# Optimization experiments

Hardware: AMD Instinct MI355X
Metric: run time of the kernel (lower is better)

The kernel has to match this reference:

```python
import jax, jax.numpy as jnp
import numpy as np

N = 50000      # num nodes
HID = 64       # hidden_dim
N2V = 64       # node2vec dim
E = 800000     # num edges
EP = 100000    # prediction edges
L = 2          # num_layers
EPS = 1e-5     # BatchNorm eps


def setup_inputs() -> dict:
    key = jax.random.key(0)
    ks = jax.random.split(key, 8)
    edge_index = jax.random.randint(ks[0], (2, E), 0, N)
    pred_edge = jax.random.randint(ks[1], (EP, 2), 0, N)
    id_emb = jax.random.normal(ks[2], (N, HID), jnp.float32) * 0.1      # learnable ID embedding
    n2v_emb = jax.random.normal(ks[3], (N, N2V), jnp.float32) * 0.1     # frozen node2vec embedding
    proj_w = jax.random.normal(ks[4], (HID + N2V, HID), jnp.float32) / np.sqrt(HID + N2V)
    proj_b = jnp.zeros((HID,), jnp.float32)
    conv_w = jax.random.normal(ks[5], (L, HID, HID), jnp.float32) / np.sqrt(HID)
    conv_b = jnp.zeros((L, HID), jnp.float32)
    bn_gamma = jnp.ones((L, HID), jnp.float32)
    bn_beta = jnp.zeros((L, HID), jnp.float32)
    return {"edge_index": edge_index, "pred_edge": pred_edge, "id_emb": id_emb,
            "n2v_emb": n2v_emb, "proj_w": proj_w, "proj_b": proj_b,
            "conv_w": conv_w, "conv_b": conv_b, "bn_gamma": bn_gamma, "bn_beta": bn_beta}


def reference(edge_index, pred_edge, id_emb, n2v_emb, proj_w, proj_b, conv_w, conv_b, bn_gamma, bn_beta):
    # input projection of concatenated embeddings: [N, HID+N2V] @ [HID+N2V, HID]
    x = jnp.concatenate([id_emb, n2v_emb], axis=1) @ proj_w + proj_b

    # GCN normalization with self-loops: norm_e = d^-1/2[src] * d^-1/2[dst]
    loops = jnp.arange(N, dtype=edge_index.dtype)
    row = jnp.concatenate([edge_index[0], loops])   # source nodes
    col = jnp.concatenate([edge_index[1], loops])   # destination nodes
    deg = jax.ops.segment_sum(jnp.ones(row.shape, x.dtype), col, num_segments=N)
    dis = jnp.where(deg > 0, jax.lax.rsqrt(deg), 0.0)
    norm = dis[row] * dis[col]                      # [E+N]

    for l in range(L):
        h = x @ conv_w[l]                                                    # [N, HID]
        agg = jax.ops.segment_sum(norm[:, None] * h[row], col, num_segments=N) + conv_b[l]
        # BatchNorm1d (training-mode batch stats over nodes)
        mu = agg.mean(axis=0)
        var = agg.var(axis=0)
        xn = (agg - mu) * jax.lax.rsqrt(var + EPS) * bn_gamma[l] + bn_beta[l]
        x = x + jax.nn.relu(xn)                                              # residual (shapes match)

    # dot-product link decoder
    z = x
    return (z[pred_edge[:, 0]] * z[pred_edge[:, 1]]).sum(axis=1)
```

## Files before the change

### kernel.cpp

```cpp
#include <hip/hip_runtime.h>

#define NN 50000
#define HID 64
#define NE 800000
#define NP 100000
#define BN_EPS 1e-5f
#define NB1 196

static inline size_t alignup(size_t x) { return (x + 255) & ~(size_t)255; }

__device__ __forceinline__ void f4fma(float a, const float4& w, float4& c) {
    c.x += a * w.x; c.y += a * w.y; c.z += a * w.z; c.w += a * w.w;
}
__device__ __forceinline__ void f4add(const float4& a, float4& c) {
    c.x += a.x; c.y += a.y; c.z += a.z; c.w += a.w;
}
__device__ __forceinline__ unsigned bfpack(float a, float b) {
    unsigned ua = __float_as_uint(a), ub = __float_as_uint(b);
    ua = (ua + 0x7fffu + ((ua >> 16) & 1u)) >> 16;
    ub = (ub + 0x7fffu + ((ub >> 16) & 1u)) >> 16;
    return ua | (ub << 16);
}
__device__ __forceinline__ float4 bf2f4(uint2 u) {
    float4 r;
    r.x = __uint_as_float(u.x << 16);
    r.y = __uint_as_float(u.x & 0xffff0000u);
    r.z = __uint_as_float(u.y << 16);
    r.w = __uint_as_float(u.y & 0xffff0000u);
    return r;
}


__global__ __launch_bounds__(256) void k_zero(int* __restrict__ cnt, float* __restrict__ sums,
                                              int* __restrict__ cursor) {
    int i = blockIdx.x * blockDim.x + threadIdx.x;
    if (i < NN) cnt[i] = 0;
    if (i < 256) sums[i] = 0.f;
    if (i == 0) *cursor = 0;
}


__global__ __launch_bounds__(256) void k_count(const int* __restrict__ col,
                                               int* __restrict__ cnt, int* __restrict__ rank) {
    int e = blockIdx.x * blockDim.x + threadIdx.x;
    if (e < NE) rank[e] = atomicAdd(&cnt[col[e]], 1);
}


__global__ __launch_bounds__(256) void k_alloc(const int* __restrict__ cnt,
                                               int* __restrict__ offs,
                                               float* __restrict__ dis,
                                               int* __restrict__ cursor) {
    __shared__ int s[256];
    __shared__ int base;
    int t = threadIdx.x;
    int i = blockIdx.x * 256 + t;
    int v = (i < NN) ? cnt[i] : 0;
    if (i < NN) dis[i] = rsqrtf((float)(v + 1));
    s[t] = v;
    __syncthreads();
    for (int off = 1; off < 256; off <<= 1) {
        int add = (t >= off) ? s[t - off] : 0;
        __syncthreads();
        s[t] += add;
        __syncthreads();
    }
    if (t == 255) base = atomicAdd(cursor, s[255]);
    __syncthreads();
    if (i < NN) offs[i] = base + s[t] - v;
}


__global__ __launch_bounds__(256) void k_fill(const int* __restrict__ row, const int* __restrict__ col,
                                              const int* __restrict__ rank, const int* __restrict__ offs,
                                              int* __restrict__ csr_src) {
    int e = blockIdx.x * blockDim.x + threadIdx.x;
    if (e >= NE) return;
    csr_src[offs[col[e]] + rank[e]] = row[e];
}


__global__ __launch_bounds__(256) void k_proj(const float* __restrict__ id_emb,
                                              const float* __restrict__ n2v,
                                              const float* __restrict__ W,
                                              const float* __restrict__ b,
                                              const float* __restrict__ dis,
                                              float* __restrict__ x,
                                              unsigned short* __restrict__ xh) {
    __shared__ float Wl[128 * 64];
    int tid = threadIdx.x;
    for (int i = tid; i < 128 * 64; i += 256) Wl[i] = W[i];
    __syncthreads();
    int sub = tid >> 4, q = tid & 15;
    const float4* W4 = (const float4*)Wl;
    const float4* id4 = (const float4*)id_emb;
    const float4* nv4 = (const float4*)n2v;
    float4* x4 = (float4*)x;
    uint2* xh2 = (uint2*)xh;
    float4 bb = ((const float4*)b)[q];
    const int ngroups = (NN + 63) / 64;
    for (int g = blockIdx.x; g < ngroups; g += gridDim.x) {
        int n0 = g * 64 + sub * 4;
        int r0 = min(n0 + 0, NN - 1), r1 = min(n0 + 1, NN - 1);
        int r2 = min(n0 + 2, NN - 1), r3 = min(n0 + 3, NN - 1);
        float4 c0 = bb, c1 = bb, c2 = bb, c3 = bb;
#pragma unroll 4
        for (int k4 = 0; k4 < 16; ++k4) {
            float4 a0 = id4[r0 * 16 + k4];
            float4 a1 = id4[r1 * 16 + k4];
            float4 a2 = id4[r2 * 16 + k4];
            float4 a3 = id4[r3 * 16 + k4];
            float4 w0 = W4[(k4 * 4 + 0) * 16 + q];
            float4 w1 = W4[(k4 * 4 + 1) * 16 + q];
            float4 w2 = W4[(k4 * 4 + 2) * 16 + q];
            float4 w3 = W4[(k4 * 4 + 3) * 16 + q];
            f4fma(a0.x, w0, c0); f4fma(a0.y, w1, c0); f4fma(a0.z, w2, c0); f4fma(a0.w, w3, c0);
            f4fma(a1.x, w0, c1); f4fma(a1.y, w1, c1); f4fma(a1.z, w2, c1); f4fma(a1.w, w3, c1);
            f4fma(a2.x, w0, c2); f4fma(a2.y, w1, c2); f4fma(a2.z, w2, c2); f4fma(a2.w, w3, c2);
            f4fma(a3.x, w0, c3); f4fma(a3.y, w1, c3); f4fma(a3.z, w2, c3); f4fma(a3.w, w3, c3);
        }
#pragma unroll 4
        for (int k4 = 0; k4 < 16; ++k4) {
            float4 a0 = nv4[r0 * 16 + k4];
            float4 a1 = nv4[r1 * 16 + k4];
            float4 a2 = nv4[r2 * 16 + k4];
            float4 a3 = nv4[r3 * 16 + k4];
            float4 w0 = W4[(k4 * 4 + 64) * 16 + q];
            float4 w1 = W4[(k4 * 4 + 65) * 16 + q];
            float4 w2 = W4[(k4 * 4 + 66) * 16 + q];
            float4 w3 = W4[(k4 * 4 + 67) * 16 + q];
            f4fma(a0.x, w0, c0); f4fma(a0.y, w1, c0); f4fma(a0.z, w2, c0); f4fma(a0.w, w3, c0);
            f4fma(a1.x, w0, c1); f4fma(a1.y, w1, c1); f4fma(a1.z, w2, c1); f4fma(a1.w, w3, c1);
            f4fma(a2.x, w0, c2); f4fma(a2.y, w1, c2); f4fma(a2.z, w2, c2); f4fma(a2.w, w3, c2);
            f4fma(a3.x, w0, c3); f4fma(a3.y, w1, c3); f4fma(a3.z, w2, c3); f4fma(a3.w, w3, c3);
        }
        if (n0 + 0 < NN) { float d = dis[n0+0]; x4[(n0+0)*16+q] = c0;
            xh2[(n0+0)*16+q] = make_uint2(bfpack(c0.x*d,c0.y*d), bfpack(c0.z*d,c0.w*d)); }
        if (n0 + 1 < NN) { float d = dis[n0+1]; x4[(n0+1)*16+q] = c1;
            xh2[(n0+1)*16+q] = make_uint2(bfpack(c1.x*d,c1.y*d), bfpack(c1.z*d,c1.w*d)); }
        if (n0 + 2 < NN) { float d = dis[n0+2]; x4[(n0+2)*16+q] = c2;
            xh2[(n0+2)*16+q] = make_uint2(bfpack(c2.x*d,c2.y*d), bfpack(c2.z*d,c2.w*d)); }
        if (n0 + 3 < NN) { float d = dis[n0+3]; x4[(n0+3)*16+q] = c3;
            xh2[(n0+3)*16+q] = make_uint2(bfpack(c3.x*d,c3.y*d), bfpack(c3.z*d,c3.w*d)); }
    }
}


__global__ __launch_bounds__(256) void k_gg(const int* __restrict__ offs,
                                            const int* __restrict__ cnt,
                                            const int* __restrict__ csr_src,
                                            const float* __restrict__ dis,
                                            const unsigned short* __restrict__ xh,
                                            unsigned short* __restrict__ th,
                                            const float* __restrict__ W,
                                            float* __restrict__ agg,
                                            float* __restrict__ sums) {
    __shared__ float Wl[64 * 64];
    __shared__ float ls0[16][64];
    __shared__ float ls1[16][64];
    int tid = threadIdx.x;
    for (int i = tid; i < 64 * 64; i += 256) Wl[i] = W[i];
    int node0 = blockIdx.x * 64;
    const uint2* xh2 = (const uint2*)xh;
    uint2* th2 = (uint2*)th;
    {
        int wave = tid >> 6, lane = tid & 63;
        int gsub = lane >> 4, q = lane & 15;
        for (int r = 0; r < 4; ++r) {
            int node = node0 + wave * 16 + r * 4 + gsub;
            if (node < NN) {
                float4 acc = make_float4(0.f, 0.f, 0.f, 0.f);
                int j = offs[node], j1 = j + cnt[node];
                for (; j + 7 < j1; j += 8) {
                    int s0 = csr_src[j],     s1 = csr_src[j + 1], s2 = csr_src[j + 2], s3 = csr_src[j + 3];
                    int s4 = csr_src[j + 4], s5 = csr_src[j + 5], s6 = csr_src[j + 6], s7 = csr_src[j + 7];
                    uint2 u0 = xh2[s0 * 16 + q];
                    uint2 u1 = xh2[s1 * 16 + q];
                    uint2 u2 = xh2[s2 * 16 + q];
                    uint2 u3 = xh2[s3 * 16 + q];
                    uint2 u4 = xh2[s4 * 16 + q];
                    uint2 u5 = xh2[s5 * 16 + q];
                    uint2 u6 = xh2[s6 * 16 + q];
                    uint2 u7 = xh2[s7 * 16 + q];
                    f4add(bf2f4(u0), acc); f4add(bf2f4(u1), acc);
                    f4add(bf2f4(u2), acc); f4add(bf2f4(u3), acc);
                    f4add(bf2f4(u4), acc); f4add(bf2f4(u5), acc);
                    f4add(bf2f4(u6), acc); f4add(bf2f4(u7), acc);
                }
                for (; j < j1; ++j) {
                    uint2 u0 = xh2[csr_src[j] * 16 + q];
                    f4add(bf2f4(u0), acc);
                }
                f4add(bf2f4(xh2[node * 16 + q]), acc);
                float di = dis[node];
                acc.x *= di; acc.y *= di; acc.z *= di; acc.w *= di;
                th2[node * 16 + q] = make_uint2(bfpack(acc.x, acc.y), bfpack(acc.z, acc.w));
            }
        }
    }
    __syncthreads();
    int sub = tid >> 4, q = tid & 15;
    const uint2* t2 = (const uint2*)th;
    const float4* W4 = (const float4*)Wl;
    float4* agg4 = (float4*)agg;
    int n0 = node0 + sub * 4;
    int r0 = min(n0 + 0, NN - 1), r1 = min(n0 + 1, NN - 1);
    int r2 = min(n0 + 2, NN - 1), r3 = min(n0 + 3, NN - 1);
    float4 c0 = make_float4(0.f,0.f,0.f,0.f), c1 = c0, c2 = c0, c3 = c0;
#pragma unroll 4
    for (int k4 = 0; k4 < 16; ++k4) {
        float4 a0 = bf2f4(t2[r0 * 16 + k4]);
        float4 a1 = bf2f4(t2[r1 * 16 + k4]);
        float4 a2 = bf2f4(t2[r2 * 16 + k4]);
        float4 a3 = bf2f4(t2[r3 * 16 + k4]);
        float4 w0 = W4[(k4 * 4 + 0) * 16 + q];
        float4 w1 = W4[(k4 * 4 + 1) * 16 + q];
        float4 w2 = W4[(k4 * 4 + 2) * 16 + q];
        float4 w3 = W4[(k4 * 4 + 3) * 16 + q];
        f4fma(a0.x, w0, c0); f4fma(a0.y, w1, c0); f4fma(a0.z, w2, c0); f4fma(a0.w, w3, c0);
        f4fma(a1.x, w0, c1); f4fma(a1.y, w1, c1); f4fma(a1.z, w2, c1); f4fma(a1.w, w3, c1);
        f4fma(a2.x, w0, c2); f4fma(a2.y, w1, c2); f4fma(a2.z, w2, c2); f4fma(a2.w, w3, c2);
        f4fma(a3.x, w0, c3); f4fma(a3.y, w1, c3); f4fma(a3.z, w2, c3); f4fma(a3.w, w3, c3);
    }
    float4 s1 = make_float4(0.f,0.f,0.f,0.f), s2 = s1;
    if (n0 + 0 < NN) { agg4[(n0 + 0) * 16 + q] = c0;
        s1.x += c0.x; s1.y += c0.y; s1.z += c0.z; s1.w += c0.w;
        s2.x += c0.x*c0.x; s2.y += c0.y*c0.y; s2.z += c0.z*c0.z; s2.w += c0.w*c0.w; }
    if (n0 + 1 < NN) { agg4[(n0 + 1) * 16 + q] = c1;
        s1.x += c1.x; s1.y += c1.y; s1.z += c1.z; s1.w += c1.w;
        s2.x += c1.x*c1.x; s2.y += c1.y*c1.y; s2.z += c1.z*c1.z; s2.w += c1.w*c1.w; }
    if (n0 + 2 < NN) { agg4[(n0 + 2) * 16 + q] = c2;
        s1.x += c2.x; s1.y += c2.y; s1.z += c2.z; s1.w += c2.w;
        s2.x += c2.x*c2.x; s2.y += c2.y*c2.y; s2.z += c2.z*c2.z; s2.w += c2.w*c2.w; }
    if (n0 + 3 < NN) { agg4[(n0 + 3) * 16 + q] = c3;
        s1.x += c3.x; s1.y += c3.y; s1.z += c3.z; s1.w += c3.w;
        s2.x += c3.x*c3.x; s2.y += c3.y*c3.y; s2.z += c3.z*c3.z; s2.w += c3.w*c3.w; }
    ls0[sub][q * 4 + 0] = s1.x; ls0[sub][q * 4 + 1] = s1.y;
    ls0[sub][q * 4 + 2] = s1.z; ls0[sub][q * 4 + 3] = s1.w;
    ls1[sub][q * 4 + 0] = s2.x; ls1[sub][q * 4 + 1] = s2.y;
    ls1[sub][q * 4 + 2] = s2.z; ls1[sub][q * 4 + 3] = s2.w;
    __syncthreads();
    if (tid < 64) {
        float a = 0.f;
#pragma unroll
        for (int r = 0; r < 16; ++r) a += ls0[r][tid];
        atomicAdd(&sums[tid], a);
    } else if (tid < 128) {
        int c = tid - 64;
        float a = 0.f;
#pragma unroll
        for (int r = 0; r < 16; ++r) a += ls1[r][c];
        atomicAdd(&sums[64 + c], a);
    }
}


__global__ __launch_bounds__(256) void k_bnupdate(const float* __restrict__ agg,
                                                  const float* __restrict__ sums,
                                                  const float* __restrict__ gamma,
                                                  const float* __restrict__ beta,
                                                  const float* __restrict__ dis,
                                                  int prescale,
                                                  float* __restrict__ x,
                                                  unsigned short* __restrict__ xh) {
    int i = blockIdx.x * blockDim.x + threadIdx.x;
    if (i >= NN * 16) return;
    int f4 = i & 15;
    const float invn = 1.0f / (float)NN;
    float4 sm = ((const float4*)sums)[f4];
    float4 sq = ((const float4*)(sums + 64))[f4];
    float4 g = ((const float4*)gamma)[f4];
    float4 be = ((const float4*)beta)[f4];
    float4 a = ((const float4*)agg)[i];
    float4 xv = ((const float4*)x)[i];
    float mu, var, rstd, xn;
    mu = sm.x * invn; var = sq.x * invn - mu * mu; rstd = rsqrtf(var + BN_EPS);
    xn = (a.x - mu) * rstd * g.x + be.x; xv.x += fmaxf(xn, 0.f);
    mu = sm.y * invn; var = sq.y * invn - mu * mu; rstd = rsqrtf(var + BN_EPS);
    xn = (a.y - mu) * rstd * g.y + be.y; xv.y += fmaxf(xn, 0.f);
    mu = sm.z * invn; var = sq.z * invn - mu * mu; rstd = rsqrtf(var + BN_EPS);
    xn = (a.z - mu) * rstd * g.z + be.z; xv.z += fmaxf(xn, 0.f);
    mu = sm.w * invn; var = sq.w * invn - mu * mu; rstd = rsqrtf(var + BN_EPS);
    xn = (a.w - mu) * rstd * g.w + be.w; xv.w += fmaxf(xn, 0.f);
    ((float4*)x)[i] = xv;
    float d = prescale ? dis[i >> 4] : 1.0f;
    ((uint2*)xh)[i] = make_uint2(bfpack(xv.x * d, xv.y * d), bfpack(xv.z * d, xv.w * d));
}


__global__ __launch_bounds__(256) void k_decode(const int* __restrict__ pred,
                                                const unsigned short* __restrict__ zh,
                                                float* __restrict__ out) {
    int gw = (blockIdx.x * blockDim.x + threadIdx.x) >> 6;
    int lane = threadIdx.x & 63;
    int sub = lane >> 4, q = lane & 15;
    int p = gw * 4 + sub;
    if (p >= NP) return;
    const uint2* z2 = (const uint2*)zh;
    int a = pred[2 * p], b = pred[2 * p + 1];
    float4 va = bf2f4(z2[a * 16 + q]);
    float4 vb = bf2f4(z2[b * 16 + q]);
    float v = va.x * vb.x + va.y * vb.y + va.z * vb.z + va.w * vb.w;
    v += __shfl_xor(v, 1);
    v += __shfl_xor(v, 2);
    v += __shfl_xor(v, 4);
    v += __shfl_xor(v, 8);
    if (q == 0) out[p] = v;
}

extern "C" void kernel_launch(void* const* d_in, const int* in_sizes, int n_in,
                              void* d_out, int out_size, void* d_ws, size_t ws_size,
                              hipStream_t stream) {
    const int* edge_index = (const int*)d_in[0];
    const int* pred       = (const int*)d_in[1];
    const float* id_emb   = (const float*)d_in[2];
    const float* n2v      = (const float*)d_in[3];
    const float* proj_w   = (const float*)d_in[4];
    const float* proj_b   = (const float*)d_in[5];
    const float* conv_w   = (const float*)d_in[6];
    const float* gamma    = (const float*)d_in[8];
    const float* beta     = (const float*)d_in[9];
    float* out = (float*)d_out;

    char* ws = (char*)d_ws;
    size_t off = 0;
    float* dis   = (float*)(ws + off); off += alignup(NN * 4);
    int* cnt     = (int*)(ws + off);   off += alignup(NN * 4);
    int* offs    = (int*)(ws + off);   off += alignup(NN * 4);
    int* rank    = (int*)(ws + off);   off += alignup((size_t)NE * 4);
    int* cursor  = (int*)(ws + off);   off += alignup(4);
    int* csr_src = (int*)(ws + off);   off += alignup((size_t)NE * 4);
    float* x     = (float*)(ws + off); off += alignup((size_t)NN * 64 * 4);
    float* agg   = (float*)(ws + off); off += alignup((size_t)NN * 64 * 4);
    unsigned short* xh = (unsigned short*)(ws + off); off += alignup((size_t)NN * 64 * 2);
    unsigned short* th = (unsigned short*)(ws + off); off += alignup((size_t)NN * 64 * 2);
    float* sums  = (float*)(ws + off);

    const int* row = edge_index;
    const int* col = edge_index + NE;

    k_zero<<<NB1, 256, 0, stream>>>(cnt, sums, cursor);
    k_count<<<(NE + 255) / 256, 256, 0, stream>>>(col, cnt, rank);
    k_alloc<<<NB1, 256, 0, stream>>>(cnt, offs, dis, cursor);
    k_fill<<<(NE + 255) / 256, 256, 0, stream>>>(row, col, rank, offs, csr_src);

    k_proj<<<512, 256, 0, stream>>>(id_emb, n2v, proj_w, proj_b, dis, x, xh);

    for (int l = 0; l < 2; ++l) {
        k_gg<<<(NN + 63) / 64, 256, 0, stream>>>(offs, cnt, csr_src, dis, xh, th,
                                                 conv_w + l * 64 * 64, agg, sums + l * 128);
        k_bnupdate<<<(NN * 16 + 255) / 256, 256, 0, stream>>>(agg, sums + l * 128, gamma + l * 64,
                                                              beta + l * 64, dis, (l == 0) ? 1 : 0, x, xh);
    }

    k_decode<<<(NP / 4 * 64 + 255) / 256, 256, 0, stream>>>(pred, xh, out);
}
```

Measured before the change: 218.3 us.

## Split fused gather-GEMM kernel into separate gather and persistent GEMM-stats kernels

The fused per-layer kernel that gathered neighbor features and then ran the 64x64 GEMM with BN statistics is split into two kernels. The gather kernel no longer loads a 16KB weight tile into shared memory, so it should reach higher occupancy for the latency-bound irregular reads. The GEMM kernel becomes a grid-stride loop over 512 blocks, which amortizes the weight load and cuts the number of atomic adds on the stats. In exchange there is an extra kernel launch per layer and the intermediate th buffer is read back from global memory instead of being consumed in the same block.

New measurement: 205.0 us. 1.07x faster.

```diff
diff --git a/kernel.cpp b/kernel.cpp
--- a/kernel.cpp
+++ b/kernel.cpp
@@ -146,95 +146,96 @@
 }
 
 
-__global__ __launch_bounds__(256) void k_gg(const int* __restrict__ offs,
-                                            const int* __restrict__ cnt,
-                                            const int* __restrict__ csr_src,
-                                            const float* __restrict__ dis,
-                                            const unsigned short* __restrict__ xh,
-                                            unsigned short* __restrict__ th,
-                                            const float* __restrict__ W,
-                                            float* __restrict__ agg,
-                                            float* __restrict__ sums) {
+__global__ __launch_bounds__(256) void k_gather(const int* __restrict__ offs,
+                                                const int* __restrict__ cnt,
+                                                const int* __restrict__ csr_src,
+                                                const float* __restrict__ dis,
+                                                const unsigned short* __restrict__ xh,
+                                                unsigned short* __restrict__ th) {
+    int gw = (blockIdx.x * blockDim.x + threadIdx.x) >> 6;
+    int lane = threadIdx.x & 63;
+    int sub = lane >> 4, q = lane & 15;
+    int node = gw * 4 + sub;
+    if (node >= NN) return;
+    const uint2* xh2 = (const uint2*)xh;
+    float4 acc = make_float4(0.f, 0.f, 0.f, 0.f);
+    int j = offs[node], j1 = j + cnt[node];
+    for (; j + 7 < j1; j += 8) {
+        int s0 = csr_src[j],     s1 = csr_src[j + 1], s2 = csr_src[j + 2], s3 = csr_src[j + 3];
+        int s4 = csr_src[j + 4], s5 = csr_src[j + 5], s6 = csr_src[j + 6], s7 = csr_src[j + 7];
+        uint2 u0 = xh2[s0 * 16 + q];
+        uint2 u1 = xh2[s1 * 16 + q];
+        uint2 u2 = xh2[s2 * 16 + q];
+        uint2 u3 = xh2[s3 * 16 + q];
+        uint2 u4 = xh2[s4 * 16 + q];
+        uint2 u5 = xh2[s5 * 16 + q];
+        uint2 u6 = xh2[s6 * 16 + q];
+        uint2 u7 = xh2[s7 * 16 + q];
+        f4add(bf2f4(u0), acc); f4add(bf2f4(u1), acc);
+        f4add(bf2f4(u2), acc); f4add(bf2f4(u3), acc);
+        f4add(bf2f4(u4), acc); f4add(bf2f4(u5), acc);
+        f4add(bf2f4(u6), acc); f4add(bf2f4(u7), acc);
+    }
+    for (; j < j1; ++j) {
+        uint2 u0 = xh2[csr_src[j] * 16 + q];
+        f4add(bf2f4(u0), acc);
+    }
+    f4add(bf2f4(xh2[node * 16 + q]), acc);
+    float di = dis[node];
+    acc.x *= di; acc.y *= di; acc.z *= di; acc.w *= di;
+    ((uint2*)th)[node * 16 + q] = make_uint2(bfpack(acc.x, acc.y), bfpack(acc.z, acc.w));
+}
+
+
+__global__ __launch_bounds__(256) void k_gemm_stats(const unsigned short* __restrict__ th,
+                                                    const float* __restrict__ W,
+                                                    float* __restrict__ agg,
+                                                    float* __restrict__ sums) {
     __shared__ float Wl[64 * 64];
     __shared__ float ls0[16][64];
     __shared__ float ls1[16][64];
     int tid = threadIdx.x;
     for (int i = tid; i < 64 * 64; i += 256) Wl[i] = W[i];
-    int node0 = blockIdx.x * 64;
-    const uint2* xh2 = (const uint2*)xh;
-    uint2* th2 = (uint2*)th;
-    {
-        int wave = tid >> 6, lane = tid & 63;
-        int gsub = lane >> 4, q = lane & 15;
-        for (int r = 0; r < 4; ++r) {
-            int node = node0 + wave * 16 + r * 4 + gsub;
-            if (node < NN) {
-                float4 acc = make_float4(0.f, 0.f, 0.f, 0.f);
-                int j = offs[node], j1 = j + cnt[node];
-                for (; j + 7 < j1; j += 8) {
-                    int s0 = csr_src[j],     s1 = csr_src[j + 1], s2 = csr_src[j + 2], s3 = csr_src[j + 3];
-                    int s4 = csr_src[j + 4], s5 = csr_src[j + 5], s6 = csr_src[j + 6], s7 = csr_src[j + 7];
-                    uint2 u0 = xh2[s0 * 16 + q];
-                    uint2 u1 = xh2[s1 * 16 + q];
-                    uint2 u2 = xh2[s2 * 16 + q];
-                    uint2 u3 = xh2[s3 * 16 + q];
-                    uint2 u4 = xh2[s4 * 16 + q];
-                    uint2 u5 = xh2[s5 * 16 + q];
-                    uint2 u6 = xh2[s6 * 16 + q];
-                    uint2 u7 = xh2[s7 * 16 + q];
-                    f4add(bf2f4(u0), acc); f4add(bf2f4(u1), acc);
-                    f4add(bf2f4(u2), acc); f4add(bf2f4(u3), acc);
-                    f4add(bf2f4(u4), acc); f4add(bf2f4(u5), acc);
-                    f4add(bf2f4(u6), acc); f4add(bf2f4(u7), acc);
-                }
-                for (; j < j1; ++j) {
-                    uint2 u0 = xh2[csr_src[j] * 16 + q];
-                    f4add(bf2f4(u0), acc);
-                }
-                f4add(bf2f4(xh2[node * 16 + q]), acc);
-                float di = dis[node];
-                acc.x *= di; acc.y *= di; acc.z *= di; acc.w *= di;
-                th2[node * 16 + q] = make_uint2(bfpack(acc.x, acc.y), bfpack(acc.z, acc.w));
-            }
-        }
-    }
     __syncthreads();
     int sub = tid >> 4, q = tid & 15;
     const uint2* t2 = (const uint2*)th;
     const float4* W4 = (const float4*)Wl;
     float4* agg4 = (float4*)agg;
-    int n0 = node0 + sub * 4;
-    int r0 = min(n0 + 0, NN - 1), r1 = min(n0 + 1, NN - 1);
-    int r2 = min(n0 + 2, NN - 1), r3 = min(n0 + 3, NN - 1);
-    float4 c0 = make_float4(0.f,0.f,0.f,0.f), c1 = c0, c2 = c0, c3 = c0;
+    float4 s1 = make_float4(0.f, 0.f, 0.f, 0.f), s2 = s1;
+    const int ngroups = (NN + 63) / 64;
+    for (int g = blockIdx.x; g < ngroups; g += gridDim.x) {
+        int n0 = g * 64 + sub * 4;
+        int r0 = min(n0 + 0, NN - 1), r1 = min(n0 + 1, NN - 1);
+        int r2 = min(n0 + 2, NN - 1), r3 = min(n0 + 3, NN - 1);
+        float4 c0 = make_float4(0.f,0.f,0.f,0.f), c1 = c0, c2 = c0, c3 = c0;
 #pragma unroll 4
-    for (int k4 = 0; k4 < 16; ++k4) {
-        float4 a0 = bf2f4(t2[r0 * 16 + k4]);
-        float4 a1 = bf2f4(t2[r1 * 16 + k4]);
-        float4 a2 = bf2f4(t2[r2 * 16 + k4]);
-        float4 a3 = bf2f4(t2[r3 * 16 + k4]);
-        float4 w0 = W4[(k4 * 4 + 0) * 16 + q];
-        float4 w1 = W4[(k4 * 4 + 1) * 16 + q];
-        float4 w2 = W4[(k4 * 4 + 2) * 16 + q];
-        float4 w3 = W4[(k4 * 4 + 3) * 16 + q];
-        f4fma(a0.x, w0, c0); f4fma(a0.y, w1, c0); f4fma(a0.z, w2, c0); f4fma(a0.w, w3, c0);
-        f4fma(a1.x, w0, c1); f4fma(a1.y, w1, c1); f4fma(a1.z, w2, c1); f4fma(a1.w, w3, c1);
-        f4fma(a2.x, w0, c2); f4fma(a2.y, w1, c2); f4fma(a2.z, w2, c2); f4fma(a2.w, w3, c2);
-        f4fma(a3.x, w0, c3); f4fma(a3.y, w1, c3); f4fma(a3.z, w2, c3); f4fma(a3.w, w3, c3);
-    }
-    float4 s1 = make_float4(0.f,0.f,0.f,0.f), s2 = s1;
-    if (n0 + 0 < NN) { agg4[(n0 + 0) * 16 + q] = c0;
-        s1.x += c0.x; s1.y += c0.y; s1.z += c0.z; s1.w += c0.w;
-        s2.x += c0.x*c0.x; s2.y += c0.y*c0.y; s2.z += c0.z*c0.z; s2.w += c0.w*c0.w; }
-    if (n0 + 1 < NN) { agg4[(n0 + 1) * 16 + q] = c1;
-        s1.x += c1.x; s1.y += c1.y; s1.z += c1.z; s1.w += c1.w;
-        s2.x += c1.x*c1.x; s2.y += c1.y*c1.y; s2.z += c1.z*c1.z; s2.w += c1.w*c1.w; }
-    if (n0 + 2 < NN) { agg4[(n0 + 2) * 16 + q] = c2;
-        s1.x += c2.x; s1.y += c2.y; s1.z += c2.z; s1.w += c2.w;
-        s2.x += c2.x*c2.x; s2.y += c2.y*c2.y; s2.z += c2.z*c2.z; s2.w += c2.w*c2.w; }
-    if (n0 + 3 < NN) { agg4[(n0 + 3) * 16 + q] = c3;
-        s1.x += c3.x; s1.y += c3.y; s1.z += c3.z; s1.w += c3.w;
-        s2.x += c3.x*c3.x; s2.y += c3.y*c3.y; s2.z += c3.z*c3.z; s2.w += c3.w*c3.w; }
+        for (int k4 = 0; k4 < 16; ++k4) {
+            float4 a0 = bf2f4(t2[r0 * 16 + k4]);
+            float4 a1 = bf2f4(t2[r1 * 16 + k4]);
+            float4 a2 = bf2f4(t2[r2 * 16 + k4]);
+            float4 a3 = bf2f4(t2[r3 * 16 + k4]);
+            float4 w0 = W4[(k4 * 4 + 0) * 16 + q];
+            float4 w1 = W4[(k4 * 4 + 1) * 16 + q];
+            float4 w2 = W4[(k4 * 4 + 2) * 16 + q];
+            float4 w3 = W4[(k4 * 4 + 3) * 16 + q];
+            f4fma(a0.x, w0, c0); f4fma(a0.y, w1, c0); f4fma(a0.z, w2, c0); f4fma(a0.w, w3, c0);
+            f4fma(a1.x, w0, c1); f4fma(a1.y, w1, c1); f4fma(a1.z, w2, c1); f4fma(a1.w, w3, c1);
+            f4fma(a2.x, w0, c2); f4fma(a2.y, w1, c2); f4fma(a2.z, w2, c2); f4fma(a2.w, w3, c2);
+            f4fma(a3.x, w0, c3); f4fma(a3.y, w1, c3); f4fma(a3.z, w2, c3); f4fma(a3.w, w3, c3);
+        }
+        if (n0 + 0 < NN) { agg4[(n0 + 0) * 16 + q] = c0;
+            s1.x += c0.x; s1.y += c0.y; s1.z += c0.z; s1.w += c0.w;
+            s2.x += c0.x*c0.x; s2.y += c0.y*c0.y; s2.z += c0.z*c0.z; s2.w += c0.w*c0.w; }
+        if (n0 + 1 < NN) { agg4[(n0 + 1) * 16 + q] = c1;
+            s1.x += c1.x; s1.y += c1.y; s1.z += c1.z; s1.w += c1.w;
+            s2.x += c1.x*c1.x; s2.y += c1.y*c1.y; s2.z += c1.z*c1.z; s2.w += c1.w*c1.w; }
+        if (n0 + 2 < NN) { agg4[(n0 + 2) * 16 + q] = c2;
+            s1.x += c2.x; s1.y += c2.y; s1.z += c2.z; s1.w += c2.w;
+            s2.x += c2.x*c2.x; s2.y += c2.y*c2.y; s2.z += c2.z*c2.z; s2.w += c2.w*c2.w; }
+        if (n0 + 3 < NN) { agg4[(n0 + 3) * 16 + q] = c3;
+            s1.x += c3.x; s1.y += c3.y; s1.z += c3.z; s1.w += c3.w;
+            s2.x += c3.x*c3.x; s2.y += c3.y*c3.y; s2.z += c3.z*c3.z; s2.w += c3.w*c3.w; }
+    }
     ls0[sub][q * 4 + 0] = s1.x; ls0[sub][q * 4 + 1] = s1.y;
     ls0[sub][q * 4 + 2] = s1.z; ls0[sub][q * 4 + 3] = s1.w;
     ls1[sub][q * 4 + 0] = s2.x; ls1[sub][q * 4 + 1] = s2.y;
@@ -347,8 +348,8 @@
     k_proj<<<512, 256, 0, stream>>>(id_emb, n2v, proj_w, proj_b, dis, x, xh);
 
     for (int l = 0; l < 2; ++l) {
-        k_gg<<<(NN + 63) / 64, 256, 0, stream>>>(offs, cnt, csr_src, dis, xh, th,
-                                                 conv_w + l * 64 * 64, agg, sums + l * 128);
+        k_gather<<<((NN + 3) / 4 * 64 + 255) / 256, 256, 0, stream>>>(offs, cnt, csr_src, dis, xh, th);
+        k_gemm_stats<<<512, 256, 0, stream>>>(th, conv_w + l * 64 * 64, agg, sums + l * 128);
         k_bnupdate<<<(NN * 16 + 255) / 256, 256, 0, stream>>>(agg, sums + l * 128, gamma + l * 64,
                                                               beta + l * 64, dis, (l == 0) ? 1 : 0, x, xh);
     }
```
